# Kernel optimization log

Measured on AMD Instinct MI355X. Metric: run time of the kernel, lower is better.

The kernel has to match this reference:

```python
import jax, jax.numpy as jnp
import numpy as np

DT = 0.1  # discretization step (matches init kwarg dt)


def setup_inputs() -> dict:
    key = jax.random.key(0)
    k1, k2, k3, k4 = jax.random.split(key, 4)
    Bsz, L, D, N = 16, 4096, 128, 64
    x = jax.random.normal(k1, (Bsz, L, D), dtype=jnp.float32)
    # torch uses torch.rand for A; shift by -N*I so A is Hurwitz and the
    # 4096-step recurrence stays numerically stable (same math, stable init).
    A = jax.random.uniform(k2, (D, N, N), dtype=jnp.float32) - float(N) * jnp.eye(N, dtype=jnp.float32)
    B = jax.random.uniform(k3, (D, N, 1), dtype=jnp.float32)
    C = jax.random.uniform(k4, (D, 1, N), dtype=jnp.float32)
    return {"x": x, "A": A, "B": B, "C": C}


def _discretize(A, B):
    # Bilinear (Tustin) transform, per channel d: [D, N, N]
    N = A.shape[-1]
    I = jnp.eye(N, dtype=A.dtype)[None, :, :]
    inv = jnp.linalg.inv(I - A * (DT / 2))
    A_bar = inv @ (I + A * (DT / 2))          # [D, N, N]
    B_bar = (inv @ B) * DT                    # [D, N, 1]
    return A_bar, B_bar


def reference(x, A, B, C):
    # x: [Bsz, L, D]; A: [D, N, N]; B: [D, N, 1]; C: [D, 1, N]
    Bsz, L, D = x.shape
    N = A.shape[-1]
    A_bar, B_bar = _discretize(A, B)
    Bb = B_bar[:, :, 0]                       # [D, N]
    Cv = C[:, 0, :]                           # [D, N]
    xs = jnp.moveaxis(x, 1, 0)                # [L, Bsz, D]
    h0 = jnp.zeros((Bsz, D, N), dtype=x.dtype)

    def step(h, x_t):
        # h_new[b,d,m] = sum_n A_bar[d,m,n] h[b,d,n] + x_t[b,d] * Bb[d,m]
        h = jnp.einsum('dmn,bdn->bdm', A_bar, h) + x_t[:, :, None] * Bb[None]
        y_t = jnp.einsum('bdn,dn->bd', h, Cv)
        return h, y_t

    _, ys = jax.lax.scan(step, h0, xs)        # ys: [L, Bsz, D]
    return jnp.moveaxis(ys, 0, 1)             # [Bsz, L, D]
```

## Files before the change

kernel.cpp:

```cpp
#include <hip/hip_runtime.h>

typedef float f4 __attribute__((ext_vector_type(4)));

#define PAD 68

#define SEED_C2 0.0251681f
#define SEED_C1 (-0.262380f)
#define SEED_C0 0.895613f

__device__ __forceinline__ void mm_acc8x4(const float* L, const float* R,
                                          int i0, int j0, float acc[32]) {
  #pragma unroll
  for (int m = 0; m < 32; ++m) acc[m] = 0.f;
  #pragma unroll
  for (int n = 0; n < 64; n += 4) {
    f4 La[8], Rb[4];
    #pragma unroll
    for (int m = 0; m < 8; ++m) La[m] = *(const f4*)&L[(i0 + m) * PAD + n];
    #pragma unroll
    for (int p = 0; p < 4; ++p) Rb[p] = *(const f4*)&R[(n + p) * PAD + j0];
    #pragma unroll
    for (int m = 0; m < 8; ++m)
      #pragma unroll
      for (int p = 0; p < 4; ++p)
        #pragma unroll
        for (int c = 0; c < 4; ++c)
          acc[m * 4 + c] += La[m][p] * Rb[p][c];
  }
}

__global__ __launch_bounds__(256) void s4_discretize(
    const float* __restrict__ Ag,
    const float* __restrict__ Bg,
    const float* __restrict__ Cg,
    float* __restrict__ Kout)
{
  __shared__ float Ms[64 * PAD];
  __shared__ float Xs[64 * PAD];
  __shared__ float Ts[64 * PAD];
  __shared__ float U16[16][PAD];
  __shared__ float Pr[4][64];
  __shared__ float Bv[64], Cv0[64], Bb[64], Cc1[64];

  const int d   = blockIdx.x;
  const int tid = threadIdx.x;
  const int i0  = (tid >> 4) << 3;
  const int j0  = (tid & 15) << 2;
  const int q   = tid >> 6;
  const int ln  = tid & 63;
  const int co  = tid >> 2;
  const int cc  = tid & 3;

  for (int idx = tid; idx < 4096; idx += 256) {
    int i = idx >> 6, j = idx & 63;
    float a = Ag[(size_t)d * 4096 + idx];
    Ms[i * PAD + j] = ((i == j) ? 1.f : 0.f) - 0.05f * a;
  }
  if (tid < 64) { Bv[tid] = Bg[d * 64 + tid]; Cv0[tid] = Cg[d * 64 + tid]; }
  __syncthreads();

  float acc[32];

  if (tid < 128) {
    mm_acc8x4(Ms, Ms, i0, j0, acc);
    #pragma unroll
    for (int m = 0; m < 8; ++m) {
      f4 mo = *(const f4*)&Ms[(i0 + m) * PAD + j0];
      f4 t;
      #pragma unroll
      for (int c = 0; c < 4; ++c)
        t[c] = SEED_C2 * acc[m*4+c] + SEED_C1 * mo[c]
             + ((i0 + m == j0 + c) ? SEED_C0 : 0.f);
      *(f4*)&Xs[(i0 + m) * PAD + j0] = t;
    }
  }
  __syncthreads();

  if (tid < 128) {
    mm_acc8x4(Ms, Xs, i0, j0, acc);
    #pragma unroll
    for (int m = 0; m < 8; ++m) {
      f4 t;
      #pragma unroll
      for (int c = 0; c < 4; ++c)
        t[c] = ((i0 + m == j0 + c) ? 2.f : 0.f) - acc[m*4+c];
      *(f4*)&Ts[(i0 + m) * PAD + j0] = t;
    }
  }
  __syncthreads();

  if (tid < 128) mm_acc8x4(Xs, Ts, i0, j0, acc);
  __syncthreads();
  if (tid < 128) {
    #pragma unroll
    for (int m = 0; m < 8; ++m) {
      f4 t = {acc[m*4+0], acc[m*4+1], acc[m*4+2], acc[m*4+3]};
      *(f4*)&Xs[(i0 + m) * PAD + j0] = t;
    }
  }
  __syncthreads();

  {
    float p = 0.f;
    #pragma unroll
    for (int m = 0; m < 16; ++m) p += Xs[ln * PAD + q * 16 + m] * Bv[q * 16 + m];
    Pr[q][ln] = p;
  }
  for (int idx = tid; idx < 4096; idx += 256) {
    int i = idx >> 6, j = idx & 63;
    Ms[i * PAD + j] = 2.f * Xs[i * PAD + j] - ((i == j) ? 1.f : 0.f);
  }
  __syncthreads();
  if (tid < 64) Bb[tid] = 0.1f * (Pr[0][tid] + Pr[1][tid] + Pr[2][tid] + Pr[3][tid]);
  __syncthreads();

  {
    float p = 0.f;
    #pragma unroll
    for (int m = 0; m < 16; ++m)
      p += Cv0[cc * 16 + m] * Ms[(cc * 16 + m) * PAD + co];
    p += __shfl_xor(p, 1);
    p += __shfl_xor(p, 2);
    if (cc == 0) Cc1[co] = p;
  }
  if (tid < 128) {
    mm_acc8x4(Ms, Ms, i0, j0, acc);
    #pragma unroll
    for (int m = 0; m < 8; ++m) {
      f4 t = {acc[m*4+0], acc[m*4+1], acc[m*4+2], acc[m*4+3]};
      *(f4*)&Ts[(i0 + m) * PAD + j0] = t;
    }
  }
  if (tid < 64) U16[0][tid] = Bb[tid];
  __syncthreads();

  for (int i = 1; i < 16; ++i) {
    const float* Arow = &Ts[co * PAD + cc * 16];
    const float* uv   = &U16[i - 1][cc * 16];
    float p = 0.f;
    #pragma unroll
    for (int j = 0; j < 4; ++j) {
      f4 a = *(const f4*)&Arow[4 * j];
      f4 u = *(const f4*)&uv[4 * j];
      p += a[0]*u[0] + a[1]*u[1] + a[2]*u[2] + a[3]*u[3];
    }
    p += __shfl_xor(p, 1);
    p += __shfl_xor(p, 2);
    if (cc == 0) U16[i][co] = p;
    __syncthreads();
  }

  {
    const int k = tid >> 3, e = tid & 7;
    const float* cvec = (k & 1) ? Cc1 : Cv0;
    const float* uvec = U16[k >> 1];
    float p = 0.f;
    #pragma unroll
    for (int j = 0; j < 8; ++j) p += cvec[e * 8 + j] * uvec[e * 8 + j];
    p += __shfl_xor(p, 1);
    p += __shfl_xor(p, 2);
    p += __shfl_xor(p, 4);
    if (e == 0) Kout[k * 128 + d] = p;
  }
}

__global__ __launch_bounds__(256, 4) void s4_conv(
    const float* __restrict__ xg,
    const float* __restrict__ Ktg,
    float* __restrict__ yg)
{
  __shared__ float xs[287 * 32];
  __shared__ float Ks[32 * 32];

  const int tid = threadIdx.y * 32 + threadIdx.x;
  const int tc  = blockIdx.x;
  const int dq  = blockIdx.y;
  const int b   = blockIdx.z;
  const int d0  = dq * 32;
  const int t0  = tc * 256;

  for (int idx = tid; idx < 1024; idx += 256)
    Ks[idx] = Ktg[(idx >> 5) * 128 + d0 + (idx & 31)];

  const float* xb = xg + (size_t)b * 4096 * 128 + d0;
  for (int idx = tid; idx < 287 * 8; idx += 256) {
    int row = idx >> 3, c4 = (idx & 7) << 2;
    int t = t0 - 31 + row;
    f4 v = {0.f, 0.f, 0.f, 0.f};
    if (t >= 0) v = *(const f4*)&xb[(size_t)t * 128 + c4];
    *(f4*)&xs[row * 32 + c4] = v;
  }
  __syncthreads();

  const int dl = threadIdx.x;
  const int g  = threadIdx.y;

  float acc[32];
  #pragma unroll
  for (int t = 0; t < 32; ++t) acc[t] = 0.f;

  float w[47];
  #pragma unroll
  for (int k0 = 0; k0 < 32; k0 += 16) {
    const int base = g * 32 + 16 - k0;
    #pragma unroll
    for (int jj = 0; jj < 47; ++jj) w[jj] = xs[(base + jj) * 32 + dl];
    #pragma unroll
    for (int k = k0; k < k0 + 16; ++k) {
      float kv = Ks[k * 32 + dl];
      #pragma unroll
      for (int t = 0; t < 32; ++t)
        acc[t] += kv * w[t + (k0 + 15 - k)];
    }
  }

  float* yb = yg + ((size_t)b * 4096 + t0 + g * 32) * 128 + d0 + dl;
  #pragma unroll
  for (int t = 0; t < 32; ++t)
    yb[(size_t)t * 128] = acc[t];
}

extern "C" void kernel_launch(void* const* d_in, const int* in_sizes, int n_in,
                              void* d_out, int out_size, void* d_ws, size_t ws_size,
                              hipStream_t stream) {
  const float* x = (const float*)d_in[0];
  const float* A = (const float*)d_in[1];
  const float* B = (const float*)d_in[2];
  const float* C = (const float*)d_in[3];
  float* y  = (float*)d_out;
  float* Kt = (float*)d_ws;

  s4_discretize<<<128, 256, 0, stream>>>(A, B, C, Kt);
  dim3 grid(16, 4, 16), block(32, 8);
  s4_conv<<<grid, block, 0, stream>>>(x, Kt, y);
}
```

Before: 115.0 us.

## Use all 256 threads for matmuls and split kernel taps into 4x8 factorization

The discretize kernel now gives each of the 256 threads a 4x4 output tile instead of using only 128 threads with 8x4 tiles, so the whole block shares the 64x64 matrix multiplies. The 32 convolution taps are rebuilt as C·A^j·(A^4)^i B with j<4 and i<8: three serial C-vector updates plus one extra squaring (A^4) cut the serial matrix-vector chain from 15 steps to 7. The global load of A and the B_bar reduction are also vectorised. The aim is a shorter latency-bound prologue kernel, paid for with one extra 64x64 matmul and a few more barrier-separated steps.

```diff
diff --git a/kernel.cpp b/kernel.cpp
--- a/kernel.cpp
+++ b/kernel.cpp
@@ -8,19 +8,19 @@
 #define SEED_C1 (-0.262380f)
 #define SEED_C0 0.895613f
 
-__device__ __forceinline__ void mm_acc8x4(const float* L, const float* R,
-                                          int i0, int j0, float acc[32]) {
-  #pragma unroll
-  for (int m = 0; m < 32; ++m) acc[m] = 0.f;
+__device__ __forceinline__ void mm_acc(const float* L, const float* R,
+                                       int i0, int j0, float acc[16]) {
+  #pragma unroll
+  for (int m = 0; m < 16; ++m) acc[m] = 0.f;
   #pragma unroll
   for (int n = 0; n < 64; n += 4) {
-    f4 La[8], Rb[4];
-    #pragma unroll
-    for (int m = 0; m < 8; ++m) La[m] = *(const f4*)&L[(i0 + m) * PAD + n];
+    f4 La[4], Rb[4];
+    #pragma unroll
+    for (int m = 0; m < 4; ++m) La[m] = *(const f4*)&L[(i0 + m) * PAD + n];
     #pragma unroll
     for (int p = 0; p < 4; ++p) Rb[p] = *(const f4*)&R[(n + p) * PAD + j0];
     #pragma unroll
-    for (int m = 0; m < 8; ++m)
+    for (int m = 0; m < 4; ++m)
       #pragma unroll
       for (int p = 0; p < 4; ++p)
         #pragma unroll
@@ -38,125 +38,143 @@
   __shared__ float Ms[64 * PAD];
   __shared__ float Xs[64 * PAD];
   __shared__ float Ts[64 * PAD];
-  __shared__ float U16[16][PAD];
-  __shared__ float Pr[4][64];
-  __shared__ float Bv[64], Cv0[64], Bb[64], Cc1[64];
+  __shared__ float C4[4][PAD];
+  __shared__ float U8[8][72];
+  __shared__ float Bv[64], Cv0[64], Bb[64];
 
   const int d   = blockIdx.x;
   const int tid = threadIdx.x;
-  const int i0  = (tid >> 4) << 3;
+  const int i0  = (tid >> 4) << 2;
   const int j0  = (tid & 15) << 2;
-  const int q   = tid >> 6;
-  const int ln  = tid & 63;
   const int co  = tid >> 2;
   const int cc  = tid & 3;
 
-  for (int idx = tid; idx < 4096; idx += 256) {
-    int i = idx >> 6, j = idx & 63;
-    float a = Ag[(size_t)d * 4096 + idx];
-    Ms[i * PAD + j] = ((i == j) ? 1.f : 0.f) - 0.05f * a;
-  }
-  if (tid < 64) { Bv[tid] = Bg[d * 64 + tid]; Cv0[tid] = Cg[d * 64 + tid]; }
-  __syncthreads();
-
-  float acc[32];
-
-  if (tid < 128) {
-    mm_acc8x4(Ms, Ms, i0, j0, acc);
-    #pragma unroll
-    for (int m = 0; m < 8; ++m) {
-      f4 mo = *(const f4*)&Ms[(i0 + m) * PAD + j0];
+  {
+    const f4* Af = (const f4*)(Ag + (size_t)d * 4096);
+    for (int v = tid; v < 1024; v += 256) {
+      int i = v >> 4, jc = (v & 15) << 2;
+      f4 a = Af[v];
       f4 t;
       #pragma unroll
       for (int c = 0; c < 4; ++c)
-        t[c] = SEED_C2 * acc[m*4+c] + SEED_C1 * mo[c]
-             + ((i0 + m == j0 + c) ? SEED_C0 : 0.f);
-      *(f4*)&Xs[(i0 + m) * PAD + j0] = t;
-    }
-  }
-  __syncthreads();
-
-  if (tid < 128) {
-    mm_acc8x4(Ms, Xs, i0, j0, acc);
-    #pragma unroll
-    for (int m = 0; m < 8; ++m) {
-      f4 t;
-      #pragma unroll
-      for (int c = 0; c < 4; ++c)
-        t[c] = ((i0 + m == j0 + c) ? 2.f : 0.f) - acc[m*4+c];
-      *(f4*)&Ts[(i0 + m) * PAD + j0] = t;
-    }
-  }
-  __syncthreads();
-
-  if (tid < 128) mm_acc8x4(Xs, Ts, i0, j0, acc);
-  __syncthreads();
-  if (tid < 128) {
-    #pragma unroll
-    for (int m = 0; m < 8; ++m) {
-      f4 t = {acc[m*4+0], acc[m*4+1], acc[m*4+2], acc[m*4+3]};
-      *(f4*)&Xs[(i0 + m) * PAD + j0] = t;
-    }
+        t[c] = ((i == jc + c) ? 1.f : 0.f) - 0.05f * a[c];
+      *(f4*)&Ms[i * PAD + jc] = t;
+    }
+  }
+  if (tid < 64) { Bv[tid] = Bg[d * 64 + tid]; Cv0[tid] = Cg[d * 64 + tid]; }
+  __syncthreads();
+
+  float acc[16];
+
+  mm_acc(Ms, Ms, i0, j0, acc);
+  #pragma unroll
+  for (int m = 0; m < 4; ++m) {
+    f4 mo = *(const f4*)&Ms[(i0 + m) * PAD + j0];
+    f4 t;
+    #pragma unroll
+    for (int c = 0; c < 4; ++c)
+      t[c] = SEED_C2 * acc[m*4+c] + SEED_C1 * mo[c]
+           + ((i0 + m == j0 + c) ? SEED_C0 : 0.f);
+    *(f4*)&Xs[(i0 + m) * PAD + j0] = t;
+  }
+  __syncthreads();
+
+  mm_acc(Ms, Xs, i0, j0, acc);
+  #pragma unroll
+  for (int m = 0; m < 4; ++m) {
+    f4 t;
+    #pragma unroll
+    for (int c = 0; c < 4; ++c)
+      t[c] = ((i0 + m == j0 + c) ? 2.f : 0.f) - acc[m*4+c];
+    *(f4*)&Ts[(i0 + m) * PAD + j0] = t;
+  }
+  __syncthreads();
+
+  mm_acc(Xs, Ts, i0, j0, acc);
+  __syncthreads();
+  #pragma unroll
+  for (int m = 0; m < 4; ++m) {
+    f4 t = {acc[m*4+0], acc[m*4+1], acc[m*4+2], acc[m*4+3]};
+    *(f4*)&Xs[(i0 + m) * PAD + j0] = t;
   }
   __syncthreads();
 
   {
     float p = 0.f;
     #pragma unroll
-    for (int m = 0; m < 16; ++m) p += Xs[ln * PAD + q * 16 + m] * Bv[q * 16 + m];
-    Pr[q][ln] = p;
-  }
-  for (int idx = tid; idx < 4096; idx += 256) {
-    int i = idx >> 6, j = idx & 63;
-    Ms[i * PAD + j] = 2.f * Xs[i * PAD + j] - ((i == j) ? 1.f : 0.f);
-  }
-  __syncthreads();
-  if (tid < 64) Bb[tid] = 0.1f * (Pr[0][tid] + Pr[1][tid] + Pr[2][tid] + Pr[3][tid]);
-  __syncthreads();
-
-  {
+    for (int j = 0; j < 4; ++j) {
+      f4 x = *(const f4*)&Xs[co * PAD + cc * 16 + 4 * j];
+      f4 b = *(const f4*)&Bv[cc * 16 + 4 * j];
+      p += x[0]*b[0] + x[1]*b[1] + x[2]*b[2] + x[3]*b[3];
+    }
+    p += __shfl_xor(p, 1);
+    p += __shfl_xor(p, 2);
+    if (cc == 0) Bb[co] = 0.1f * p;
+  }
+  for (int v = tid; v < 1024; v += 256) {
+    int i = v >> 4, jc = (v & 15) << 2;
+    f4 x = *(const f4*)&Xs[i * PAD + jc];
+    f4 t;
+    #pragma unroll
+    for (int c = 0; c < 4; ++c)
+      t[c] = 2.f * x[c] - ((i == jc + c) ? 1.f : 0.f);
+    *(f4*)&Ms[i * PAD + jc] = t;
+  }
+  if (tid < 64) C4[0][tid] = Cv0[tid];
+  __syncthreads();
+
+  for (int j = 1; j < 4; ++j) {
     float p = 0.f;
     #pragma unroll
     for (int m = 0; m < 16; ++m)
-      p += Cv0[cc * 16 + m] * Ms[(cc * 16 + m) * PAD + co];
-    p += __shfl_xor(p, 1);
-    p += __shfl_xor(p, 2);
-    if (cc == 0) Cc1[co] = p;
-  }
-  if (tid < 128) {
-    mm_acc8x4(Ms, Ms, i0, j0, acc);
-    #pragma unroll
-    for (int m = 0; m < 8; ++m) {
-      f4 t = {acc[m*4+0], acc[m*4+1], acc[m*4+2], acc[m*4+3]};
-      *(f4*)&Ts[(i0 + m) * PAD + j0] = t;
-    }
-  }
-  if (tid < 64) U16[0][tid] = Bb[tid];
-  __syncthreads();
-
-  for (int i = 1; i < 16; ++i) {
-    const float* Arow = &Ts[co * PAD + cc * 16];
-    const float* uv   = &U16[i - 1][cc * 16];
+      p += C4[j - 1][cc * 16 + m] * Ms[(cc * 16 + m) * PAD + co];
+    p += __shfl_xor(p, 1);
+    p += __shfl_xor(p, 2);
+    if (cc == 0) C4[j][co] = p;
+    __syncthreads();
+  }
+
+  mm_acc(Ms, Ms, i0, j0, acc);
+  #pragma unroll
+  for (int m = 0; m < 4; ++m) {
+    f4 t = {acc[m*4+0], acc[m*4+1], acc[m*4+2], acc[m*4+3]};
+    *(f4*)&Ts[(i0 + m) * PAD + j0] = t;
+  }
+  __syncthreads();
+
+  mm_acc(Ts, Ts, i0, j0, acc);
+  #pragma unroll
+  for (int m = 0; m < 4; ++m) {
+    f4 t = {acc[m*4+0], acc[m*4+1], acc[m*4+2], acc[m*4+3]};
+    *(f4*)&Xs[(i0 + m) * PAD + j0] = t;
+  }
+  if (tid < 64) U8[0][tid] = Bb[tid];
+  __syncthreads();
+
+  for (int i = 1; i < 8; ++i) {
     float p = 0.f;
     #pragma unroll
     for (int j = 0; j < 4; ++j) {
-      f4 a = *(const f4*)&Arow[4 * j];
-      f4 u = *(const f4*)&uv[4 * j];
+      f4 a = *(const f4*)&Xs[co * PAD + cc * 16 + 4 * j];
+      f4 u = *(const f4*)&U8[i - 1][cc * 16 + 4 * j];
       p += a[0]*u[0] + a[1]*u[1] + a[2]*u[2] + a[3]*u[3];
     }
     p += __shfl_xor(p, 1);
     p += __shfl_xor(p, 2);
-    if (cc == 0) U16[i][co] = p;
+    if (cc == 0) U8[i][co] = p;
     __syncthreads();
   }
 
   {
     const int k = tid >> 3, e = tid & 7;
-    const float* cvec = (k & 1) ? Cc1 : Cv0;
-    const float* uvec = U16[k >> 1];
-    float p = 0.f;
-    #pragma unroll
-    for (int j = 0; j < 8; ++j) p += cvec[e * 8 + j] * uvec[e * 8 + j];
+    const float* cvec = C4[k & 3];
+    const float* uvec = U8[k >> 2];
+    f4 c0 = *(const f4*)&cvec[e * 8];
+    f4 c1 = *(const f4*)&cvec[e * 8 + 4];
+    f4 u0 = *(const f4*)&uvec[e * 8];
+    f4 u1 = *(const f4*)&uvec[e * 8 + 4];
+    float p = c0[0]*u0[0] + c0[1]*u0[1] + c0[2]*u0[2] + c0[3]*u0[3]
+            + c1[0]*u1[0] + c1[1]*u1[1] + c1[2]*u1[2] + c1[3]*u1[3];
     p += __shfl_xor(p, 1);
     p += __shfl_xor(p, 2);
     p += __shfl_xor(p, 4);
```

Result: faster. 111.2 us (-3.3%).
